# Kernel tuning notes

Hardware: AMD Instinct MI355X
Metric: run time of the kernel (lower is better)

## Reference

```python
import jax, jax.numpy as jnp
import numpy as np
from jax import lax

V, E, Q, D = 100000, 300, 64, 4096
K = 5
NEG_SLOPE = 0.01


def setup_inputs() -> dict:
    key = jax.random.key(0)
    ks = jax.random.split(key, 16)
    return {
        "question": jax.random.randint(ks[0], (Q,), 0, V),
        "doc1": jax.random.randint(ks[1], (D,), 0, V),
        "doc2": jax.random.randint(ks[2], (D,), 0, V),
        "doc1_sim": jax.random.uniform(ks[3], (D, Q), dtype=jnp.float32),
        "doc2_sim": jax.random.uniform(ks[4], (D, Q), dtype=jnp.float32),
        "gaf": jax.random.normal(ks[5], (4,), dtype=jnp.float32),
        "baf": jax.random.normal(ks[6], (4,), dtype=jnp.float32),
        "emb": jax.random.normal(ks[7], (V, E), dtype=jnp.float32) * 0.1,
        "idf": jax.random.uniform(ks[8], (V, 1), dtype=jnp.float32) * 10.0,
        "conv_w": jax.random.normal(ks[9], (E, E, 3), dtype=jnp.float32) * (1.0 / np.sqrt(3 * E)),
        "conv_b": jax.random.normal(ks[10], (E,), dtype=jnp.float32) * 0.01,
        "qw_w": jax.random.normal(ks[11], (1, E + 1), dtype=jnp.float32) * (1.0 / np.sqrt(E + 1)),
        "qw_b": jax.random.normal(ks[12], (1,), dtype=jnp.float32) * 0.01,
        "lin1_w": jax.random.normal(ks[13], (8, 6), dtype=jnp.float32) * (1.0 / np.sqrt(6)),
        "lin2_w": jax.random.normal(ks[14], (1, 8), dtype=jnp.float32) * (1.0 / np.sqrt(8)),
        "out_w": jax.random.normal(ks[15], (1, 5), dtype=jnp.float32) * (1.0 / np.sqrt(5)),
    }


def _leaky(x):
    return jnp.where(x >= 0, x, NEG_SLOPE * x)


def _conv_residual(x, w, b):
    # x: [L, E]. Torch Conv1d(E,E,3,padding=2) followed by slice [1:L+1] is a
    # centered SAME conv; activation applied before the residual add.
    y = lax.conv_general_dilated(x.T[None], w, (1,), [(1, 1)],
                                 dimension_numbers=("NCW", "OIW", "NCW"))
    y = y[0] + b[:, None]            # [E, L]
    return _leaky(y).T + x           # [L, E]


def _cosine(A, B):
    # A: [Q, E], B: [L, E] -> [Q, L]
    num = A @ B.T
    den = jnp.linalg.norm(A, axis=-1)[:, None] * jnp.linalg.norm(B, axis=-1)[None, :]
    return num / den


def _kmax_pool(sim):
    # sim: [Q, L] -> [Q, 2] = (max, mean of top-K)
    top = lax.top_k(sim, K)[0]       # descending [Q, K]
    return jnp.stack([top[:, 0], jnp.mean(top, axis=-1)], axis=-1)


def _get_output(pooled_list, q_weights, lin1_w, lin2_w):
    temp = jnp.concatenate(pooled_list, axis=-1)     # [Q, 6]
    lo = _leaky(temp @ lin1_w.T) @ lin2_w.T          # [Q, 1]
    lo = lo[:, 0] * q_weights
    return jnp.sum(lo) / lo.shape[0]


def reference(question, doc1, doc2, doc1_sim, doc2_sim, gaf, baf,
              emb, idf, conv_w, conv_b, qw_w, qw_b, lin1_w, lin2_w, out_w):
    q_emb = emb[question]            # [Q, E]
    d1_emb = emb[doc1]               # [D, E]
    d2_emb = emb[doc2]

    sim_ins_d1 = _cosine(q_emb, d1_emb)
    sim_ins_d2 = _cosine(q_emb, d2_emb)

    q_conv = _conv_residual(q_emb, conv_w, conv_b)
    d1_conv = _conv_residual(d1_emb, conv_w, conv_b)
    d2_conv = _conv_residual(d2_emb, conv_w, conv_b)

    sim_sen_d1 = _cosine(q_conv, d1_conv)
    sim_sen_d2 = _cosine(q_conv, d2_conv)

    sim_oh_d1 = doc1_sim.T           # [Q, D]
    sim_oh_d2 = doc2_sim.T

    p_oh_d1, p_ins_d1, p_sen_d1 = _kmax_pool(sim_oh_d1), _kmax_pool(sim_ins_d1), _kmax_pool(sim_sen_d1)
    p_oh_d2, p_ins_d2, p_sen_d2 = _kmax_pool(sim_oh_d2), _kmax_pool(sim_ins_d2), _kmax_pool(sim_sen_d2)

    q_idfs = idf[question]           # [Q, 1]
    qw = jnp.concatenate([q_conv, q_idfs], axis=-1) @ qw_w.T + qw_b  # [Q, 1]
    q_weights = jax.nn.softmax(qw[:, 0], axis=-1)

    doc1_emit = _get_output([p_oh_d1, p_ins_d1, p_sen_d1], q_weights, lin1_w, lin2_w)
    doc2_emit = _get_output([p_oh_d2, p_ins_d2, p_sen_d2], q_weights, lin1_w, lin2_w)

    good_feats = jnp.concatenate([gaf, doc1_emit[None]])  # [5]
    bad_feats = jnp.concatenate([baf, doc2_emit[None]])
    good_out = out_w @ good_feats                          # [1]
    bad_out = out_w @ bad_feats

    loss1 = jnp.mean(jnp.maximum(0.0, -(good_out - bad_out) + 1.0))
    return (loss1, good_out, bad_out, loss1, loss1)
```

## Files before the change

### kernel.cpp

```cpp
#include <hip/hip_runtime.h>
#include <math.h>

#define EE 300
#define KP 320
#define LDSW 328
#define QQ 64
#define DD 4096
#define NEG 0.01f

typedef __attribute__((ext_vector_type(8))) short short8;
typedef __attribute__((ext_vector_type(4))) float f32x4;
typedef unsigned short ushort_t;

__device__ inline ushort_t f2bf(float f) {
  unsigned u = __builtin_bit_cast(unsigned, f);
  u += 0x7fff + ((u >> 16) & 1);
  return (ushort_t)(u >> 16);
}
__device__ inline float bf2f(ushort_t h) {
  return __builtin_bit_cast(float, (unsigned)h << 16);
}

#define GATHER_ROWS (66 + 4098 + 4098)
#define GATHER_BLOCKS ((GATHER_ROWS + 3) / 4)
#define WT_BLOCKS 143
#define TR_BLOCKS 128
#define ZERO_BLOCKS 9
#define PREP_BLOCKS (GATHER_BLOCKS + WT_BLOCKS + TR_BLOCKS + ZERO_BLOCKS)

__global__ __launch_bounds__(256) void prep(
    const float* __restrict__ emb, const int* __restrict__ question,
    const int* __restrict__ doc1, const int* __restrict__ doc2,
    const float* __restrict__ conv_w,
    const float* __restrict__ doc1_sim, const float* __restrict__ doc2_sim,
    ushort_t* __restrict__ qbe, ushort_t* __restrict__ d1be, ushort_t* __restrict__ d2be,
    ushort_t* __restrict__ qbc, ushort_t* __restrict__ d1bc, ushort_t* __restrict__ d2bc,
    ushort_t* __restrict__ wt2,
    float* __restrict__ ohT1, float* __restrict__ ohT2,
    float* __restrict__ nq2, float* __restrict__ nd12, float* __restrict__ nd22,
    float* __restrict__ acc_zero_base) {
  __shared__ float tilebuf[64][65];
  int b = blockIdx.x;
  int tid = threadIdx.x;
  if (b < GATHER_BLOCKS) {
    int w = tid >> 6, lane = tid & 63;
    int g = b * 4 + w;
    int t, row;
    if (g < 66)             { t = 0; row = g; }
    else if (g < 66 + 4098) { t = 1; row = g - 66; }
    else if (g < GATHER_ROWS) { t = 2; row = g - 66 - 4098; }
    else return;
    const int* idx = t == 0 ? question : (t == 1 ? doc1 : doc2);
    int L = t == 0 ? QQ : DD;
    ushort_t* be = t == 0 ? qbe : (t == 1 ? d1be : d2be);
    ushort_t* bc = t == 0 ? qbc : (t == 1 ? d1bc : d2bc);
    float* nrm2 = t == 0 ? nq2 : (t == 1 ? nd12 : nd22);
    if (row == 0 || row == L + 1) {
      for (int i = lane; i < KP; i += 64) be[(size_t)row * KP + i] = 0;
      return;
    }
    int r = row - 1;
    const float* src = emb + (size_t)idx[r] * EE;
    float ss = 0.f;
    for (int i = lane; i < EE; i += 64) {
      float v = src[i];
      be[(size_t)row * KP + i] = f2bf(v);
      ss += v * v;
    }
    for (int i = EE + lane; i < KP; i += 64) {
      be[(size_t)row * KP + i] = 0;
      bc[(size_t)r * KP + i] = 0;
    }
    #pragma unroll
    for (int o = 32; o; o >>= 1) ss += __shfl_xor(ss, o);
    if (lane == 0) nrm2[r] = ss;
  } else if (b < GATHER_BLOCKS + WT_BLOCKS) {
    int f = (b - GATHER_BLOCKS) * 4 + (tid >> 6);
    if (f >= 570) return;
    int lane = tid & 63;
    int ks = f % 10, n = (f / 10) % 19, tap = f / 190;
    int o = n * 16 + (lane & 15);
    int kbase = ks * 32 + (lane >> 4) * 8;
    ushort_t* dst = wt2 + (size_t)f * 512 + lane * 8;
    #pragma unroll
    for (int e = 0; e < 8; ++e) {
      int k = kbase + e;
      float v = (o < EE && k < EE) ? conv_w[((size_t)o * EE + k) * 3 + tap] : 0.f;
      dst[e] = f2bf(v);
    }
  } else if (b < GATHER_BLOCKS + WT_BLOCKS + TR_BLOCKS) {
    int idx = b - (GATHER_BLOCKS + WT_BLOCKS);
    int srcsel = idx >> 6, tile = idx & 63;
    const float* in = srcsel ? doc2_sim : doc1_sim;
    float* outT = srcsel ? ohT2 : ohT1;
    int c = tid & 63, rq = tid >> 6;
    #pragma unroll 4
    for (int i = 0; i < 16; ++i) {
      int r = i * 4 + rq;
      tilebuf[r][c] = in[(size_t)(tile * 64 + r) * QQ + c];
    }
    __syncthreads();
    #pragma unroll 4
    for (int i = 0; i < 16; ++i) {
      int q = i * 4 + rq;
      outT[(size_t)q * DD + tile * 64 + c] = tilebuf[c][q];
    }
  } else {
    int i0 = (b - (GATHER_BLOCKS + WT_BLOCKS + TR_BLOCKS)) * 1024 + tid;
    #pragma unroll
    for (int j = 0; j < 4; ++j) {
      int i = i0 + j * 256;
      if (i < 8320) acc_zero_base[i] = 0.f;
    }
  }
}

__global__ __launch_bounds__(256) void conv_mfma(
    const ushort_t* __restrict__ wt2, const float* __restrict__ bias,
    const float* __restrict__ qw_w,
    const ushort_t* __restrict__ qbe, const ushort_t* __restrict__ d1be,
    const ushort_t* __restrict__ d2be,
    ushort_t* __restrict__ qbc, ushort_t* __restrict__ d1bc,
    ushort_t* __restrict__ d2bc,
    float* __restrict__ nqc2, float* __restrict__ nd1c2, float* __restrict__ nd2c2,
    float* __restrict__ qwacc) {
  __shared__ ushort_t lds[34 * LDSW];
  int bx = blockIdx.x;
  int t, m0, yh;
  if (bx < 4) { t = 0; m0 = (bx >> 1) * 32; yh = bx & 1; }
  else {
    int i = bx - 4;
    t = 1 + (i >> 8);
    int j = i & 255;
    m0 = (j >> 1) * 32; yh = j & 1;
  }
  const ushort_t* be = t == 0 ? qbe : (t == 1 ? d1be : d2be);
  ushort_t* bc = t == 0 ? qbc : (t == 1 ? d1bc : d2bc);
  float* nc2 = t == 0 ? nqc2 : (t == 1 ? nd1c2 : nd2c2);
  int tid = threadIdx.x;
  for (int s = tid; s < 34 * 40; s += 256) {
    int row = s / 40, col = s - row * 40;
    *(short8*)(&lds[row * LDSW + col * 8]) =
        *(const short8*)(be + (size_t)(m0 + row) * KP + col * 8);
  }
  __syncthreads();
  int w = tid >> 6, lane = tid & 63, mrow = lane & 15, g = lane >> 4;
  int nstart, ncnt;
  if (yh == 0) { nstart = (w < 2) ? 3 * w : 2 * w + 2; ncnt = (w < 2) ? 3 : 2; }
  else         { nstart = (w == 0) ? 10 : 2 * w + 11;  ncnt = (w == 0) ? 3 : 2; }
  f32x4 acc[3][2];
  #pragma unroll
  for (int j = 0; j < 3; ++j)
    #pragma unroll
    for (int h = 0; h < 2; ++h) acc[j][h] = (f32x4){0.f, 0.f, 0.f, 0.f};

  for (int tap = 0; tap < 3; ++tap) {
    const ushort_t* alo = &lds[(mrow + tap) * LDSW + g * 8];
    #pragma unroll
    for (int ks = 0; ks < 10; ++ks) {
      short8 a0 = *(const short8*)(alo + ks * 32);
      short8 a1 = *(const short8*)(alo + 16 * LDSW + ks * 32);
      #pragma unroll
      for (int j = 0; j < 3; ++j) {
        if (j < ncnt) {
          short8 bfr = *(const short8*)(wt2 +
              (size_t)((tap * 19 + nstart + j) * 10 + ks) * 512 + lane * 8);
          acc[j][0] = __builtin_amdgcn_mfma_f32_16x16x32_bf16(a0, bfr, acc[j][0], 0, 0, 0);
          acc[j][1] = __builtin_amdgcn_mfma_f32_16x16x32_bf16(a1, bfr, acc[j][1], 0, 0, 0);
        }
      }
    }
  }
  float ss[2][4] = {{0.f,0.f,0.f,0.f},{0.f,0.f,0.f,0.f}};
  float yq[2][4] = {{0.f,0.f,0.f,0.f},{0.f,0.f,0.f,0.f}};
  #pragma unroll
  for (int j = 0; j < 3; ++j) {
    if (j < ncnt) {
      int col = (nstart + j) * 16 + mrow;
      if (col < EE) {
        float bcol = bias[col];
        float qwc = (t == 0) ? qw_w[col] : 0.f;
        #pragma unroll
        for (int h = 0; h < 2; ++h) {
          #pragma unroll
          for (int r = 0; r < 4; ++r) {
            int lrow = h * 16 + g * 4 + r;
            float y = acc[j][h][r] + bcol;
            y = (y >= 0.f) ? y : NEG * y;
            y += bf2f(lds[(1 + lrow) * LDSW + col]);
            bc[(size_t)(m0 + lrow) * KP + col] = f2bf(y);
            ss[h][r] += y * y;
            if (t == 0) yq[h][r] += y * qwc;
          }
        }
      }
    }
  }
  #pragma unroll
  for (int h = 0; h < 2; ++h) {
    #pragma unroll
    for (int r = 0; r < 4; ++r) {
      float s = ss[h][r];
      s += __shfl_xor(s, 1); s += __shfl_xor(s, 2);
      s += __shfl_xor(s, 4); s += __shfl_xor(s, 8);
      if (mrow == 0) atomicAdd(&nc2[m0 + h * 16 + g * 4 + r], s);
      if (t == 0) {
        float sq = yq[h][r];
        sq += __shfl_xor(sq, 1); sq += __shfl_xor(sq, 2);
        sq += __shfl_xor(sq, 4); sq += __shfl_xor(sq, 8);
        if (mrow == 0) atomicAdd(&qwacc[m0 + h * 16 + g * 4 + r], sq);
      }
    }
  }
}

__global__ __launch_bounds__(256) void sim_mfma(
    const ushort_t* __restrict__ qbe, const ushort_t* __restrict__ d1be,
    const ushort_t* __restrict__ d2be,
    const ushort_t* __restrict__ qbc, const ushort_t* __restrict__ d1bc,
    const ushort_t* __restrict__ d2bc,
    const float* __restrict__ nq2, const float* __restrict__ nd12,
    const float* __restrict__ nd22, const float* __restrict__ nqc2,
    const float* __restrict__ nd1c2, const float* __restrict__ nd2c2,
    float* __restrict__ sims) {
  __shared__ ushort_t lds[32 * LDSW];
  int s = blockIdx.y;
  const ushort_t* A = (s < 2) ? qbe + KP : qbc;
  const ushort_t* B = s == 0 ? d1be + KP : s == 1 ? d2be + KP : s == 2 ? d1bc : d2bc;
  const float* na2 = (s < 2) ? nq2 : nqc2;
  const float* nb2 = s == 0 ? nd12 : s == 1 ? nd22 : s == 2 ? nd1c2 : nd2c2;
  float* out = sims + (size_t)s * QQ * DD;
  int l0 = blockIdx.x * 32;
  int tid = threadIdx.x;
  for (int i = tid; i < 32 * 40; i += 256) {
    int row = i / 40, col = i - row * 40;
    *(short8*)(&lds[row * LDSW + col * 8]) =
        *(const short8*)(B + (size_t)(l0 + row) * KP + col * 8);
  }
  __syncthreads();
  int w = tid >> 6, lane = tid & 63, mrow = lane & 15, g = lane >> 4;
  f32x4 acc[2];
  acc[0] = (f32x4){0.f, 0.f, 0.f, 0.f};
  acc[1] = (f32x4){0.f, 0.f, 0.f, 0.f};
  const ushort_t* arow = A + (size_t)(w * 16 + mrow) * KP + g * 8;
  #pragma unroll
  for (int ks = 0; ks < 10; ++ks) {
    short8 a = *(const short8*)(arow + ks * 32);
    #pragma unroll
    for (int n = 0; n < 2; ++n) {
      short8 bfr = *(const short8*)(&lds[(n * 16 + mrow) * LDSW + g * 8 + ks * 32]);
      acc[n] = __builtin_amdgcn_mfma_f32_16x16x32_bf16(a, bfr, acc[n], 0, 0, 0);
    }
  }
  #pragma unroll
  for (int n = 0; n < 2; ++n) {
    int l = l0 + n * 16 + mrow;
    float inb = rsqrtf(nb2[l]);
    #pragma unroll
    for (int r = 0; r < 4; ++r) {
      int q = w * 16 + g * 4 + r;
      out[(size_t)q * DD + l] = acc[n][r] * rsqrtf(na2[q]) * inb;
    }
  }
}

__device__ inline void top5_insert(float* t, float v) {
  if (v > t[4]) {
    t[4] = v;
    #pragma unroll
    for (int j = 4; j > 0; --j) {
      if (t[j] > t[j - 1]) { float tmp = t[j]; t[j] = t[j - 1]; t[j - 1] = tmp; }
    }
  }
}

__global__ __launch_bounds__(256) void kmax_pool(
    const float* __restrict__ ohT1, const float* __restrict__ ohT2,
    const float* __restrict__ sims, float* __restrict__ pool) {
  int q = blockIdx.x, src = blockIdx.y;
  int tid = threadIdx.x;
  const size_t QD = (size_t)QQ * DD;
  const float* base;
  switch (src) {
    case 0: base = ohT1; break;
    case 1: base = sims + 0 * QD; break;
    case 2: base = sims + 2 * QD; break;
    case 3: base = ohT2; break;
    case 4: base = sims + 1 * QD; break;
    default: base = sims + 3 * QD; break;
  }
  const float* row = base + (size_t)q * DD;
  float t5[5];
  #pragma unroll
  for (int j = 0; j < 5; ++j) t5[j] = -1e30f;
  for (int l = tid; l < DD; l += 256) top5_insert(t5, row[l]);
  __shared__ float ls[256][5];
  #pragma unroll
  for (int j = 0; j < 5; ++j) ls[tid][j] = t5[j];
  __syncthreads();
  for (int step = 128; step >= 1; step >>= 1) {
    if (tid < step) {
      float a[5], c[5], m[5];
      #pragma unroll
      for (int j = 0; j < 5; ++j) { a[j] = ls[tid][j]; c[j] = ls[tid + step][j]; }
      int ia = 0, ib = 0;
      #pragma unroll
      for (int j = 0; j < 5; ++j) m[j] = (a[ia] >= c[ib]) ? a[ia++] : c[ib++];
      #pragma unroll
      for (int j = 0; j < 5; ++j) ls[tid][j] = m[j];
    }
    __syncthreads();
  }
  if (tid == 0) {
    float mx = ls[0][0];
    float sm = 0.f;
    #pragma unroll
    for (int j = 0; j < 5; ++j) sm += ls[0][j];
    pool[((size_t)src * QQ + q) * 2 + 0] = mx;
    pool[((size_t)src * QQ + q) * 2 + 1] = sm * 0.2f;
  }
}

__global__ void final_kernel(
    const float* __restrict__ qwacc, const float* __restrict__ idf,
    const int* __restrict__ question, const float* __restrict__ qw_w,
    const float* __restrict__ qw_b, const float* __restrict__ pool,
    const float* __restrict__ lin1_w, const float* __restrict__ lin2_w,
    const float* __restrict__ out_w, const float* __restrict__ gaf,
    const float* __restrict__ baf, float* __restrict__ out5) {
  int q = threadIdx.x;
  float s = qwacc[q] + qw_b[0] + idf[question[q]] * qw_w[EE];
  float m = s;
  #pragma unroll
  for (int o = 32; o; o >>= 1) m = fmaxf(m, __shfl_xor(m, o));
  float e = expf(s - m);
  float se = e;
  #pragma unroll
  for (int o = 32; o; o >>= 1) se += __shfl_xor(se, o);
  float qwgt = e / se;

  float emit[2];
  for (int doc = 0; doc < 2; ++doc) {
    float temp[6];
    #pragma unroll
    for (int j = 0; j < 3; ++j) {
      temp[2 * j]     = pool[(((size_t)doc * 3 + j) * QQ + q) * 2 + 0];
      temp[2 * j + 1] = pool[(((size_t)doc * 3 + j) * QQ + q) * 2 + 1];
    }
    float lo = 0.f;
    #pragma unroll
    for (int r = 0; r < 8; ++r) {
      float h = 0.f;
      #pragma unroll
      for (int c = 0; c < 6; ++c) h += lin1_w[r * 6 + c] * temp[c];
      h = (h >= 0.f) ? h : NEG * h;
      lo += lin2_w[r] * h;
    }
    lo *= qwgt;
    #pragma unroll
    for (int o = 32; o; o >>= 1) lo += __shfl_xor(lo, o);
    emit[doc] = lo / (float)QQ;
  }
  if (q == 0) {
    float good = out_w[0] * gaf[0] + out_w[1] * gaf[1] + out_w[2] * gaf[2] +
                 out_w[3] * gaf[3] + out_w[4] * emit[0];
    float bad  = out_w[0] * baf[0] + out_w[1] * baf[1] + out_w[2] * baf[2] +
                 out_w[3] * baf[3] + out_w[4] * emit[1];
    float l1 = fmaxf(0.f, -(good - bad) + 1.f);
    out5[0] = l1; out5[1] = good; out5[2] = bad; out5[3] = l1; out5[4] = l1;
  }
}

extern "C" void kernel_launch(void* const* d_in, const int* in_sizes, int n_in,
                              void* d_out, int out_size, void* d_ws, size_t ws_size,
                              hipStream_t stream) {
  (void)in_sizes; (void)n_in; (void)out_size; (void)ws_size;
  const int* question   = (const int*)d_in[0];
  const int* doc1       = (const int*)d_in[1];
  const int* doc2       = (const int*)d_in[2];
  const float* doc1_sim = (const float*)d_in[3];
  const float* doc2_sim = (const float*)d_in[4];
  const float* gaf      = (const float*)d_in[5];
  const float* baf      = (const float*)d_in[6];
  const float* emb      = (const float*)d_in[7];
  const float* idf      = (const float*)d_in[8];
  const float* conv_w   = (const float*)d_in[9];
  const float* conv_b   = (const float*)d_in[10];
  const float* qw_w     = (const float*)d_in[11];
  const float* qw_b     = (const float*)d_in[12];
  const float* lin1_w   = (const float*)d_in[13];
  const float* lin2_w   = (const float*)d_in[14];
  const float* out_w    = (const float*)d_in[15];
  float* out = (float*)d_out;

  char* p = (char*)d_ws;
  ushort_t* qbe  = (ushort_t*)p; p += (size_t)(QQ + 2) * KP * 2;
  ushort_t* d1be = (ushort_t*)p; p += (size_t)(DD + 2) * KP * 2;
  ushort_t* d2be = (ushort_t*)p; p += (size_t)(DD + 2) * KP * 2;
  ushort_t* qbc  = (ushort_t*)p; p += (size_t)QQ * KP * 2;
  ushort_t* d1bc = (ushort_t*)p; p += (size_t)DD * KP * 2;
  ushort_t* d2bc = (ushort_t*)p; p += (size_t)DD * KP * 2;
  ushort_t* wt2  = (ushort_t*)p; p += (size_t)570 * 512 * 2;
  float* sims = (float*)p; p += (size_t)4 * QQ * DD * 4;
  float* ohT1 = (float*)p; p += (size_t)QQ * DD * 4;
  float* ohT2 = (float*)p; p += (size_t)QQ * DD * 4;
  float* nq2  = (float*)p; p += QQ * 4;
  float* nd12 = (float*)p; p += DD * 4;
  float* nd22 = (float*)p; p += DD * 4;
  float* nqc2  = (float*)p; p += QQ * 4;
  float* nd1c2 = (float*)p; p += DD * 4;
  float* nd2c2 = (float*)p; p += DD * 4;
  float* qwacc = (float*)p; p += QQ * 4;
  float* pool  = (float*)p; p += 6 * QQ * 2 * 4;

  prep<<<PREP_BLOCKS, 256, 0, stream>>>(
      emb, question, doc1, doc2, conv_w, doc1_sim, doc2_sim,
      qbe, d1be, d2be, qbc, d1bc, d2bc, wt2, ohT1, ohT2,
      nq2, nd12, nd22, nqc2);

  conv_mfma<<<516, 256, 0, stream>>>(
      wt2, conv_b, qw_w, qbe, d1be, d2be, qbc, d1bc, d2bc,
      nqc2, nd1c2, nd2c2, qwacc);

  sim_mfma<<<dim3(DD / 32, 4), 256, 0, stream>>>(
      qbe, d1be, d2be, qbc, d1bc, d2bc,
      nq2, nd12, nd22, nqc2, nd1c2, nd2c2, sims);

  kmax_pool<<<dim3(QQ, 6), 256, 0, stream>>>(ohT1, ohT2, sims, pool);

  final_kernel<<<1, 64, 0, stream>>>(qwacc, idf, question, qw_w, qw_b, pool,
                                     lin1_w, lin2_w, out_w, gaf, baf, out);
}
```

Before: 62.10 us.

## Fuse embedding gather into conv kernel and fold final reduction into kmax pool

Embedding gather and bf16 conversion now happen inside the conv kernel, which loads the halo rows straight into LDS, so the separate prep pass and its round trip through global memory go away. Each conv block now covers all output columns, and its per-row norms are reduced through LDS instead of global atomics. The one-hot similarity transpose is dropped: kmax reads doc_sim with strided access instead. The final kernel is merged into kmax through a last-block atomic counter. This removes launches and intermediate traffic, at the cost of fewer conv blocks (less parallelism) and uncoalesced strided reads in kmax.

```diff
diff --git a/kernel.cpp b/kernel.cpp
--- a/kernel.cpp
+++ b/kernel.cpp
@@ -21,136 +21,92 @@
   return __builtin_bit_cast(float, (unsigned)h << 16);
 }
 
-#define GATHER_ROWS (66 + 4098 + 4098)
-#define GATHER_BLOCKS ((GATHER_ROWS + 3) / 4)
-#define WT_BLOCKS 143
-#define TR_BLOCKS 128
-#define ZERO_BLOCKS 9
-#define PREP_BLOCKS (GATHER_BLOCKS + WT_BLOCKS + TR_BLOCKS + ZERO_BLOCKS)
-
-__global__ __launch_bounds__(256) void prep(
+__global__ __launch_bounds__(256) void wtk(const float* __restrict__ w,
+                                           ushort_t* __restrict__ wt2,
+                                           unsigned* __restrict__ cnt) {
+  if (blockIdx.x == 0 && threadIdx.x == 0) *cnt = 0u;
+  int f = blockIdx.x * 4 + (threadIdx.x >> 6);
+  if (f >= 570) return;
+  int lane = threadIdx.x & 63;
+  int ks = f % 10, n = (f / 10) % 19, tap = f / 190;
+  int o = n * 16 + (lane & 15);
+  int kbase = ks * 32 + (lane >> 4) * 8;
+  ushort_t* dst = wt2 + (size_t)f * 512 + lane * 8;
+  #pragma unroll
+  for (int e = 0; e < 8; ++e) {
+    int k = kbase + e;
+    float v = (o < EE && k < EE) ? w[((size_t)o * EE + k) * 3 + tap] : 0.f;
+    dst[e] = f2bf(v);
+  }
+}
+
+__global__ __launch_bounds__(256) void gconv(
     const float* __restrict__ emb, const int* __restrict__ question,
     const int* __restrict__ doc1, const int* __restrict__ doc2,
-    const float* __restrict__ conv_w,
-    const float* __restrict__ doc1_sim, const float* __restrict__ doc2_sim,
+    const ushort_t* __restrict__ wt2, const float* __restrict__ conv_b,
+    const float* __restrict__ qw_w,
     ushort_t* __restrict__ qbe, ushort_t* __restrict__ d1be, ushort_t* __restrict__ d2be,
     ushort_t* __restrict__ qbc, ushort_t* __restrict__ d1bc, ushort_t* __restrict__ d2bc,
-    ushort_t* __restrict__ wt2,
-    float* __restrict__ ohT1, float* __restrict__ ohT2,
     float* __restrict__ nq2, float* __restrict__ nd12, float* __restrict__ nd22,
-    float* __restrict__ acc_zero_base) {
-  __shared__ float tilebuf[64][65];
-  int b = blockIdx.x;
-  int tid = threadIdx.x;
-  if (b < GATHER_BLOCKS) {
-    int w = tid >> 6, lane = tid & 63;
-    int g = b * 4 + w;
-    int t, row;
-    if (g < 66)             { t = 0; row = g; }
-    else if (g < 66 + 4098) { t = 1; row = g - 66; }
-    else if (g < GATHER_ROWS) { t = 2; row = g - 66 - 4098; }
-    else return;
-    const int* idx = t == 0 ? question : (t == 1 ? doc1 : doc2);
-    int L = t == 0 ? QQ : DD;
-    ushort_t* be = t == 0 ? qbe : (t == 1 ? d1be : d2be);
-    ushort_t* bc = t == 0 ? qbc : (t == 1 ? d1bc : d2bc);
-    float* nrm2 = t == 0 ? nq2 : (t == 1 ? nd12 : nd22);
-    if (row == 0 || row == L + 1) {
-      for (int i = lane; i < KP; i += 64) be[(size_t)row * KP + i] = 0;
-      return;
-    }
-    int r = row - 1;
-    const float* src = emb + (size_t)idx[r] * EE;
-    float ss = 0.f;
-    for (int i = lane; i < EE; i += 64) {
-      float v = src[i];
-      be[(size_t)row * KP + i] = f2bf(v);
-      ss += v * v;
-    }
-    for (int i = EE + lane; i < KP; i += 64) {
-      be[(size_t)row * KP + i] = 0;
-      bc[(size_t)r * KP + i] = 0;
-    }
-    #pragma unroll
-    for (int o = 32; o; o >>= 1) ss += __shfl_xor(ss, o);
-    if (lane == 0) nrm2[r] = ss;
-  } else if (b < GATHER_BLOCKS + WT_BLOCKS) {
-    int f = (b - GATHER_BLOCKS) * 4 + (tid >> 6);
-    if (f >= 570) return;
-    int lane = tid & 63;
-    int ks = f % 10, n = (f / 10) % 19, tap = f / 190;
-    int o = n * 16 + (lane & 15);
-    int kbase = ks * 32 + (lane >> 4) * 8;
-    ushort_t* dst = wt2 + (size_t)f * 512 + lane * 8;
-    #pragma unroll
-    for (int e = 0; e < 8; ++e) {
-      int k = kbase + e;
-      float v = (o < EE && k < EE) ? conv_w[((size_t)o * EE + k) * 3 + tap] : 0.f;
-      dst[e] = f2bf(v);
-    }
-  } else if (b < GATHER_BLOCKS + WT_BLOCKS + TR_BLOCKS) {
-    int idx = b - (GATHER_BLOCKS + WT_BLOCKS);
-    int srcsel = idx >> 6, tile = idx & 63;
-    const float* in = srcsel ? doc2_sim : doc1_sim;
-    float* outT = srcsel ? ohT2 : ohT1;
-    int c = tid & 63, rq = tid >> 6;
-    #pragma unroll 4
-    for (int i = 0; i < 16; ++i) {
-      int r = i * 4 + rq;
-      tilebuf[r][c] = in[(size_t)(tile * 64 + r) * QQ + c];
-    }
-    __syncthreads();
-    #pragma unroll 4
-    for (int i = 0; i < 16; ++i) {
-      int q = i * 4 + rq;
-      outT[(size_t)q * DD + tile * 64 + c] = tilebuf[c][q];
-    }
-  } else {
-    int i0 = (b - (GATHER_BLOCKS + WT_BLOCKS + TR_BLOCKS)) * 1024 + tid;
-    #pragma unroll
-    for (int j = 0; j < 4; ++j) {
-      int i = i0 + j * 256;
-      if (i < 8320) acc_zero_base[i] = 0.f;
-    }
-  }
-}
-
-__global__ __launch_bounds__(256) void conv_mfma(
-    const ushort_t* __restrict__ wt2, const float* __restrict__ bias,
-    const float* __restrict__ qw_w,
-    const ushort_t* __restrict__ qbe, const ushort_t* __restrict__ d1be,
-    const ushort_t* __restrict__ d2be,
-    ushort_t* __restrict__ qbc, ushort_t* __restrict__ d1bc,
-    ushort_t* __restrict__ d2bc,
     float* __restrict__ nqc2, float* __restrict__ nd1c2, float* __restrict__ nd2c2,
     float* __restrict__ qwacc) {
   __shared__ ushort_t lds[34 * LDSW];
+  __shared__ float normbuf[4][32];
+  __shared__ float qwbuf[4][32];
   int bx = blockIdx.x;
-  int t, m0, yh;
-  if (bx < 4) { t = 0; m0 = (bx >> 1) * 32; yh = bx & 1; }
-  else {
-    int i = bx - 4;
-    t = 1 + (i >> 8);
-    int j = i & 255;
-    m0 = (j >> 1) * 32; yh = j & 1;
-  }
-  const ushort_t* be = t == 0 ? qbe : (t == 1 ? d1be : d2be);
+  int t, m0;
+  if (bx < 2)        { t = 0; m0 = bx * 32; }
+  else if (bx < 130) { t = 1; m0 = (bx - 2) * 32; }
+  else               { t = 2; m0 = (bx - 130) * 32; }
+  int L = t == 0 ? QQ : DD;
+  const int* idx = t == 0 ? question : (t == 1 ? doc1 : doc2);
+  ushort_t* be = t == 0 ? qbe : (t == 1 ? d1be : d2be);
   ushort_t* bc = t == 0 ? qbc : (t == 1 ? d1bc : d2bc);
+  float* ne2 = t == 0 ? nq2 : (t == 1 ? nd12 : nd22);
   float* nc2 = t == 0 ? nqc2 : (t == 1 ? nd1c2 : nd2c2);
-  int tid = threadIdx.x;
-  for (int s = tid; s < 34 * 40; s += 256) {
-    int row = s / 40, col = s - row * 40;
-    *(short8*)(&lds[row * LDSW + col * 8]) =
-        *(const short8*)(be + (size_t)(m0 + row) * KP + col * 8);
-  }
-  __syncthreads();
-  int w = tid >> 6, lane = tid & 63, mrow = lane & 15, g = lane >> 4;
-  int nstart, ncnt;
-  if (yh == 0) { nstart = (w < 2) ? 3 * w : 2 * w + 2; ncnt = (w < 2) ? 3 : 2; }
-  else         { nstart = (w == 0) ? 10 : 2 * w + 11;  ncnt = (w == 0) ? 3 : 2; }
-  f32x4 acc[3][2];
-  #pragma unroll
-  for (int j = 0; j < 3; ++j)
+  int tid = threadIdx.x, wv = tid >> 6, lane = tid & 63;
+
+  #pragma unroll
+  for (int it = 0; it < 9; ++it) {
+    int rl = wv + it * 4;
+    if (rl < 34) {
+      int gr = m0 - 1 + rl;
+      if (gr >= 0 && gr < L) {
+        const float* src = emb + (size_t)idx[gr] * EE;
+        float ss = 0.f;
+        ushort_t hb[5];
+        #pragma unroll
+        for (int c = 0; c < 5; ++c) {
+          int i = lane + c * 64;
+          if (i < EE) {
+            float v = src[i];
+            hb[c] = f2bf(v);
+            ss += v * v;
+          } else {
+            hb[c] = 0;
+          }
+          lds[rl * LDSW + i] = hb[c];
+        }
+        if (rl >= 1 && rl <= 32) {
+          #pragma unroll
+          for (int c = 0; c < 5; ++c) be[(size_t)gr * KP + lane + c * 64] = hb[c];
+          #pragma unroll
+          for (int o = 32; o; o >>= 1) ss += __shfl_xor(ss, o);
+          if (lane == 0) ne2[gr] = ss;
+        }
+      } else {
+        #pragma unroll
+        for (int c = 0; c < 5; ++c) lds[rl * LDSW + lane + c * 64] = 0;
+      }
+    }
+  }
+  __syncthreads();
+
+  int nstart = wv * 5, ncnt = (wv == 3) ? 4 : 5;
+  int mrow = lane & 15, g = lane >> 4;
+  f32x4 acc[5][2];
+  #pragma unroll
+  for (int j = 0; j < 5; ++j)
     #pragma unroll
     for (int h = 0; h < 2; ++h) acc[j][h] = (f32x4){0.f, 0.f, 0.f, 0.f};
 
@@ -161,7 +117,7 @@
       short8 a0 = *(const short8*)(alo + ks * 32);
       short8 a1 = *(const short8*)(alo + 16 * LDSW + ks * 32);
       #pragma unroll
-      for (int j = 0; j < 3; ++j) {
+      for (int j = 0; j < 5; ++j) {
         if (j < ncnt) {
           short8 bfr = *(const short8*)(wt2 +
               (size_t)((tap * 19 + nstart + j) * 10 + ks) * 512 + lane * 8);
@@ -171,14 +127,18 @@
       }
     }
   }
-  float ss[2][4] = {{0.f,0.f,0.f,0.f},{0.f,0.f,0.f,0.f}};
+  for (int i = tid; i < 32 * 20; i += 256) {
+    int row = i / 20, col = EE + i % 20;
+    bc[(size_t)(m0 + row) * KP + col] = 0;
+  }
+  float ssn[2][4] = {{0.f,0.f,0.f,0.f},{0.f,0.f,0.f,0.f}};
   float yq[2][4] = {{0.f,0.f,0.f,0.f},{0.f,0.f,0.f,0.f}};
   #pragma unroll
-  for (int j = 0; j < 3; ++j) {
+  for (int j = 0; j < 5; ++j) {
     if (j < ncnt) {
       int col = (nstart + j) * 16 + mrow;
       if (col < EE) {
-        float bcol = bias[col];
+        float bcol = conv_b[col];
         float qwc = (t == 0) ? qw_w[col] : 0.f;
         #pragma unroll
         for (int h = 0; h < 2; ++h) {
@@ -189,8 +149,8 @@
             y = (y >= 0.f) ? y : NEG * y;
             y += bf2f(lds[(1 + lrow) * LDSW + col]);
             bc[(size_t)(m0 + lrow) * KP + col] = f2bf(y);
-            ss[h][r] += y * y;
-            if (t == 0) yq[h][r] += y * qwc;
+            ssn[h][r] += y * y;
+            yq[h][r] += y * qwc;
           }
         }
       }
@@ -200,17 +160,23 @@
   for (int h = 0; h < 2; ++h) {
     #pragma unroll
     for (int r = 0; r < 4; ++r) {
-      float s = ss[h][r];
+      float s = ssn[h][r];
       s += __shfl_xor(s, 1); s += __shfl_xor(s, 2);
       s += __shfl_xor(s, 4); s += __shfl_xor(s, 8);
-      if (mrow == 0) atomicAdd(&nc2[m0 + h * 16 + g * 4 + r], s);
-      if (t == 0) {
-        float sq = yq[h][r];
-        sq += __shfl_xor(sq, 1); sq += __shfl_xor(sq, 2);
-        sq += __shfl_xor(sq, 4); sq += __shfl_xor(sq, 8);
-        if (mrow == 0) atomicAdd(&qwacc[m0 + h * 16 + g * 4 + r], sq);
-      }
-    }
+      float sq = yq[h][r];
+      sq += __shfl_xor(sq, 1); sq += __shfl_xor(sq, 2);
+      sq += __shfl_xor(sq, 4); sq += __shfl_xor(sq, 8);
+      if (mrow == 0) {
+        normbuf[wv][h * 16 + g * 4 + r] = s;
+        qwbuf[wv][h * 16 + g * 4 + r] = sq;
+      }
+    }
+  }
+  __syncthreads();
+  if (tid < 32) {
+    nc2[m0 + tid] = normbuf[0][tid] + normbuf[1][tid] + normbuf[2][tid] + normbuf[3][tid];
+    if (t == 0)
+      qwacc[m0 + tid] = qwbuf[0][tid] + qwbuf[1][tid] + qwbuf[2][tid] + qwbuf[3][tid];
   }
 }
 
@@ -225,8 +191,8 @@
     float* __restrict__ sims) {
   __shared__ ushort_t lds[32 * LDSW];
   int s = blockIdx.y;
-  const ushort_t* A = (s < 2) ? qbe + KP : qbc;
-  const ushort_t* B = s == 0 ? d1be + KP : s == 1 ? d2be + KP : s == 2 ? d1bc : d2bc;
+  const ushort_t* A = (s < 2) ? qbe : qbc;
+  const ushort_t* B = s == 0 ? d1be : s == 1 ? d2be : s == 2 ? d1bc : d2bc;
   const float* na2 = (s < 2) ? nq2 : nqc2;
   const float* nb2 = s == 0 ? nd12 : s == 1 ? nd22 : s == 2 ? nd1c2 : nd2c2;
   float* out = sims + (size_t)s * QQ * DD;
@@ -238,11 +204,11 @@
         *(const short8*)(B + (size_t)(l0 + row) * KP + col * 8);
   }
   __syncthreads();
-  int w = tid >> 6, lane = tid & 63, mrow = lane & 15, g = lane >> 4;
+  int wv = tid >> 6, lane = tid & 63, mrow = lane & 15, g = lane >> 4;
   f32x4 acc[2];
   acc[0] = (f32x4){0.f, 0.f, 0.f, 0.f};
   acc[1] = (f32x4){0.f, 0.f, 0.f, 0.f};
-  const ushort_t* arow = A + (size_t)(w * 16 + mrow) * KP + g * 8;
+  const ushort_t* arow = A + (size_t)(wv * 16 + mrow) * KP + g * 8;
   #pragma unroll
   for (int ks = 0; ks < 10; ++ks) {
     short8 a = *(const short8*)(arow + ks * 32);
@@ -258,7 +224,7 @@
     float inb = rsqrtf(nb2[l]);
     #pragma unroll
     for (int r = 0; r < 4; ++r) {
-      int q = w * 16 + g * 4 + r;
+      int q = wv * 16 + g * 4 + r;
       out[(size_t)q * DD + l] = acc[n][r] * rsqrtf(na2[q]) * inb;
     }
   }
@@ -268,33 +234,38 @@
   if (v > t[4]) {
     t[4] = v;
     #pragma unroll
-    for (int j = 4; j > 0; --j) {
+    for (int j = 4; j > 0; --j)
       if (t[j] > t[j - 1]) { float tmp = t[j]; t[j] = t[j - 1]; t[j - 1] = tmp; }
-    }
-  }
-}
-
-__global__ __launch_bounds__(256) void kmax_pool(
-    const float* __restrict__ ohT1, const float* __restrict__ ohT2,
-    const float* __restrict__ sims, float* __restrict__ pool) {
-  int q = blockIdx.x, src = blockIdx.y;
+  }
+}
+
+__global__ __launch_bounds__(256) void kmaxf(
+    const float* __restrict__ d1sim, const float* __restrict__ d2sim,
+    const float* __restrict__ sims, float* __restrict__ pool,
+    unsigned* __restrict__ cnt,
+    const float* __restrict__ qwacc, const float* __restrict__ idf,
+    const int* __restrict__ question, const float* __restrict__ qw_w,
+    const float* __restrict__ qw_b, const float* __restrict__ lin1_w,
+    const float* __restrict__ lin2_w, const float* __restrict__ out_w,
+    const float* __restrict__ gaf, const float* __restrict__ baf,
+    float* __restrict__ out5) {
+  __shared__ float ls[256][5];
+  __shared__ int islast;
+  int q = blockIdx.x & 63, src = blockIdx.x >> 6;
   int tid = threadIdx.x;
   const size_t QD = (size_t)QQ * DD;
-  const float* base;
-  switch (src) {
-    case 0: base = ohT1; break;
-    case 1: base = sims + 0 * QD; break;
-    case 2: base = sims + 2 * QD; break;
-    case 3: base = ohT2; break;
-    case 4: base = sims + 1 * QD; break;
-    default: base = sims + 3 * QD; break;
-  }
-  const float* row = base + (size_t)q * DD;
   float t5[5];
   #pragma unroll
   for (int j = 0; j < 5; ++j) t5[j] = -1e30f;
-  for (int l = tid; l < DD; l += 256) top5_insert(t5, row[l]);
-  __shared__ float ls[256][5];
+  if (src == 0) {
+    for (int l = tid; l < DD; l += 256) top5_insert(t5, d1sim[(size_t)l * QQ + q]);
+  } else if (src == 3) {
+    for (int l = tid; l < DD; l += 256) top5_insert(t5, d2sim[(size_t)l * QQ + q]);
+  } else {
+    int sidx = src == 1 ? 0 : src == 2 ? 2 : src == 4 ? 1 : 3;
+    const float* row = sims + sidx * QD + (size_t)q * DD;
+    for (int l = tid; l < DD; l += 256) top5_insert(t5, row[l]);
+  }
   #pragma unroll
   for (int j = 0; j < 5; ++j) ls[tid][j] = t5[j];
   __syncthreads();
@@ -318,56 +289,55 @@
     for (int j = 0; j < 5; ++j) sm += ls[0][j];
     pool[((size_t)src * QQ + q) * 2 + 0] = mx;
     pool[((size_t)src * QQ + q) * 2 + 1] = sm * 0.2f;
-  }
-}
-
-__global__ void final_kernel(
-    const float* __restrict__ qwacc, const float* __restrict__ idf,
-    const int* __restrict__ question, const float* __restrict__ qw_w,
-    const float* __restrict__ qw_b, const float* __restrict__ pool,
-    const float* __restrict__ lin1_w, const float* __restrict__ lin2_w,
-    const float* __restrict__ out_w, const float* __restrict__ gaf,
-    const float* __restrict__ baf, float* __restrict__ out5) {
-  int q = threadIdx.x;
-  float s = qwacc[q] + qw_b[0] + idf[question[q]] * qw_w[EE];
-  float m = s;
-  #pragma unroll
-  for (int o = 32; o; o >>= 1) m = fmaxf(m, __shfl_xor(m, o));
-  float e = expf(s - m);
-  float se = e;
-  #pragma unroll
-  for (int o = 32; o; o >>= 1) se += __shfl_xor(se, o);
-  float qwgt = e / se;
-
-  float emit[2];
-  for (int doc = 0; doc < 2; ++doc) {
-    float temp[6];
-    #pragma unroll
-    for (int j = 0; j < 3; ++j) {
-      temp[2 * j]     = pool[(((size_t)doc * 3 + j) * QQ + q) * 2 + 0];
-      temp[2 * j + 1] = pool[(((size_t)doc * 3 + j) * QQ + q) * 2 + 1];
-    }
-    float lo = 0.f;
-    #pragma unroll
-    for (int r = 0; r < 8; ++r) {
-      float h = 0.f;
-      #pragma unroll
-      for (int c = 0; c < 6; ++c) h += lin1_w[r * 6 + c] * temp[c];
-      h = (h >= 0.f) ? h : NEG * h;
-      lo += lin2_w[r] * h;
-    }
-    lo *= qwgt;
-    #pragma unroll
-    for (int o = 32; o; o >>= 1) lo += __shfl_xor(lo, o);
-    emit[doc] = lo / (float)QQ;
-  }
-  if (q == 0) {
-    float good = out_w[0] * gaf[0] + out_w[1] * gaf[1] + out_w[2] * gaf[2] +
-                 out_w[3] * gaf[3] + out_w[4] * emit[0];
-    float bad  = out_w[0] * baf[0] + out_w[1] * baf[1] + out_w[2] * baf[2] +
-                 out_w[3] * baf[3] + out_w[4] * emit[1];
-    float l1 = fmaxf(0.f, -(good - bad) + 1.f);
-    out5[0] = l1; out5[1] = good; out5[2] = bad; out5[3] = l1; out5[4] = l1;
+    __threadfence();
+    unsigned old = atomicAdd(cnt, 1u);
+    islast = (old == 383u) ? 1 : 0;
+  }
+  __syncthreads();
+  if (islast) {
+    __threadfence();
+    if (tid < 64) {
+      int qq = tid;
+      float s = qwacc[qq] + qw_b[0] + idf[question[qq]] * qw_w[EE];
+      float m = s;
+      #pragma unroll
+      for (int o = 32; o; o >>= 1) m = fmaxf(m, __shfl_xor(m, o));
+      float e = expf(s - m);
+      float se = e;
+      #pragma unroll
+      for (int o = 32; o; o >>= 1) se += __shfl_xor(se, o);
+      float qwgt = e / se;
+      float emit[2];
+      for (int doc = 0; doc < 2; ++doc) {
+        float temp[6];
+        #pragma unroll
+        for (int j = 0; j < 3; ++j) {
+          temp[2 * j]     = pool[(((size_t)doc * 3 + j) * QQ + qq) * 2 + 0];
+          temp[2 * j + 1] = pool[(((size_t)doc * 3 + j) * QQ + qq) * 2 + 1];
+        }
+        float lo = 0.f;
+        #pragma unroll
+        for (int r = 0; r < 8; ++r) {
+          float h = 0.f;
+          #pragma unroll
+          for (int c = 0; c < 6; ++c) h += lin1_w[r * 6 + c] * temp[c];
+          h = (h >= 0.f) ? h : NEG * h;
+          lo += lin2_w[r] * h;
+        }
+        lo *= qwgt;
+        #pragma unroll
+        for (int o = 32; o; o >>= 1) lo += __shfl_xor(lo, o);
+        emit[doc] = lo / (float)QQ;
+      }
+      if (qq == 0) {
+        float good = out_w[0] * gaf[0] + out_w[1] * gaf[1] + out_w[2] * gaf[2] +
+                     out_w[3] * gaf[3] + out_w[4] * emit[0];
+        float bad  = out_w[0] * baf[0] + out_w[1] * baf[1] + out_w[2] * baf[2] +
+                     out_w[3] * baf[3] + out_w[4] * emit[1];
+        float l1 = fmaxf(0.f, -(good - bad) + 1.f);
+        out5[0] = l1; out5[1] = good; out5[2] = bad; out5[3] = l1; out5[4] = l1;
+      }
+    }
   }
 }
 
@@ -394,40 +364,36 @@
   float* out = (float*)d_out;
 
   char* p = (char*)d_ws;
-  ushort_t* qbe  = (ushort_t*)p; p += (size_t)(QQ + 2) * KP * 2;
-  ushort_t* d1be = (ushort_t*)p; p += (size_t)(DD + 2) * KP * 2;
-  ushort_t* d2be = (ushort_t*)p; p += (size_t)(DD + 2) * KP * 2;
+  ushort_t* qbe  = (ushort_t*)p; p += (size_t)QQ * KP * 2;
+  ushort_t* d1be = (ushort_t*)p; p += (size_t)DD * KP * 2;
+  ushort_t* d2be = (ushort_t*)p; p += (size_t)DD * KP * 2;
   ushort_t* qbc  = (ushort_t*)p; p += (size_t)QQ * KP * 2;
   ushort_t* d1bc = (ushort_t*)p; p += (size_t)DD * KP * 2;
   ushort_t* d2bc = (ushort_t*)p; p += (size_t)DD * KP * 2;
   ushort_t* wt2  = (ushort_t*)p; p += (size_t)570 * 512 * 2;
-  float* sims = (float*)p; p += (size_t)4 * QQ * DD * 4;
-  float* ohT1 = (float*)p; p += (size_t)QQ * DD * 4;
-  float* ohT2 = (float*)p; p += (size_t)QQ * DD * 4;
-  float* nq2  = (float*)p; p += QQ * 4;
-  float* nd12 = (float*)p; p += DD * 4;
-  float* nd22 = (float*)p; p += DD * 4;
+  float* sims  = (float*)p; p += (size_t)4 * QQ * DD * 4;
+  float* nq2   = (float*)p; p += QQ * 4;
+  float* nd12  = (float*)p; p += DD * 4;
+  float* nd22  = (float*)p; p += DD * 4;
   float* nqc2  = (float*)p; p += QQ * 4;
   float* nd1c2 = (float*)p; p += DD * 4;
   float* nd2c2 = (float*)p; p += DD * 4;
   float* qwacc = (float*)p; p += QQ * 4;
   float* pool  = (float*)p; p += 6 * QQ * 2 * 4;
-
-  prep<<<PREP_BLOCKS, 256, 0, stream>>>(
-      emb, question, doc1, doc2, conv_w, doc1_sim, doc2_sim,
-      qbe, d1be, d2be, qbc, d1bc, d2bc, wt2, ohT1, ohT2,
-      nq2, nd12, nd22, nqc2);
-
-  conv_mfma<<<516, 256, 0, stream>>>(
-      wt2, conv_b, qw_w, qbe, d1be, d2be, qbc, d1bc, d2bc,
-      nqc2, nd1c2, nd2c2, qwacc);
+  unsigned* cnt = (unsigned*)p; p += 4;
+
+  wtk<<<143, 256, 0, stream>>>(conv_w, wt2, cnt);
+
+  gconv<<<258, 256, 0, stream>>>(
+      emb, question, doc1, doc2, wt2, conv_b, qw_w,
+      qbe, d1be, d2be, qbc, d1bc, d2bc,
+      nq2, nd12, nd22, nqc2, nd1c2, nd2c2, qwacc);
 
   sim_mfma<<<dim3(DD / 32, 4), 256, 0, stream>>>(
       qbe, d1be, d2be, qbc, d1bc, d2bc,
       nq2, nd12, nd22, nqc2, nd1c2, nd2c2, sims);
 
-  kmax_pool<<<dim3(QQ, 6), 256, 0, stream>>>(ohT1, ohT2, sims, pool);
-
-  final_kernel<<<1, 64, 0, stream>>>(qwacc, idf, question, qw_w, qw_b, pool,
-                                     lin1_w, lin2_w, out_w, gaf, baf, out);
-}
+  kmaxf<<<384, 256, 0, stream>>>(
+      doc1_sim, doc2_sim, sims, pool, cnt,
+      qwacc, idf, question, qw_w, qw_b, lin1_w, lin2_w, out_w, gaf, baf, out);
+}
```

After: 75.94 us. 22.3% more time.
